# Performance work log

Hardware: AMD Instinct MI355X
Metric: run time of the kernel (lower is better)

The kernel has to match this reference:

```python
import jax, jax.numpy as jnp
import numpy as np

# Mamba2 defaults: d_model=256, d_state=64, d_conv=4, expand=2, headdim=64, ngroups=1
D_MODEL = 256
NB = 2            # num_blocks
D_STATE = 64
D_CONV = 4
D_INNER = 2 * D_MODEL          # 512
HEADDIM = 64
NHEADS = D_INNER // HEADDIM    # 8
CONV_DIM = D_INNER + 2 * D_STATE           # 640
D_IN_PROJ = 2 * D_INNER + 2 * D_STATE + NHEADS  # 1160
EPS = 1e-5


def setup_inputs() -> dict:
    key = jax.random.key(0)
    ks = jax.random.split(key, 10)
    x = jax.random.normal(ks[0], (8, 32, 32, D_MODEL), dtype=jnp.float32)
    in_proj_w = jax.random.normal(ks[1], (NB, D_IN_PROJ, D_MODEL), dtype=jnp.float32) * 0.02
    conv_w = jax.random.normal(ks[2], (NB, CONV_DIM, 1, D_CONV), dtype=jnp.float32) * 0.2
    conv_b = jax.random.normal(ks[3], (NB, CONV_DIM), dtype=jnp.float32) * 0.02
    dt_bias = jax.random.normal(ks[4], (NB, NHEADS), dtype=jnp.float32) * 0.5
    # A_log = log(A), A ~ U[1,16) as in mamba2 init
    A_log = jnp.log(jax.random.uniform(ks[5], (NB, NHEADS), minval=1.0, maxval=16.0, dtype=jnp.float32))
    D = jax.random.normal(ks[6], (NB, NHEADS), dtype=jnp.float32) * 0.1 + 1.0
    norm_w = jnp.ones((NB, D_INNER), dtype=jnp.float32)
    out_proj_w = jax.random.normal(ks[7], (NB, D_MODEL, D_INNER), dtype=jnp.float32) * 0.02
    return {"x": x, "in_proj_w": in_proj_w, "conv_w": conv_w, "conv_b": conv_b,
            "dt_bias": dt_bias, "A_log": A_log, "D": D, "norm_w": norm_w,
            "out_proj_w": out_proj_w}


def _mamba2_block(h, wi, cw, cb, dtb, a_log, d_skip, nw, wo):
    B, L, _ = h.shape
    zxbcdt = jnp.einsum('blc,pc->blp', h, wi)                 # (B,L,1160)
    z = zxbcdt[..., :D_INNER]                                 # (B,L,512)
    xBC = zxbcdt[..., D_INNER:D_INNER + CONV_DIM]             # (B,L,640)
    dt = jax.nn.softplus(zxbcdt[..., -NHEADS:] + dtb)         # (B,L,8)

    # causal depthwise conv1d, kernel 4, left pad 3
    xBC = jax.lax.conv_general_dilated(
        xBC.swapaxes(1, 2), cw, window_strides=(1,), padding=[(D_CONV - 1, 0)],
        dimension_numbers=('NCH', 'OIH', 'NCH'), feature_group_count=CONV_DIM)
    xBC = jax.nn.silu((xBC + cb[None, :, None]).swapaxes(1, 2))  # (B,L,640)

    xs = xBC[..., :D_INNER].reshape(B, L, NHEADS, HEADDIM)    # (B,L,h,p)
    Bm = xBC[..., D_INNER:D_INNER + D_STATE]                  # (B,L,s) ngroups=1
    Cm = xBC[..., D_INNER + D_STATE:]                         # (B,L,s)

    A = -jnp.exp(a_log)                                       # (h,)
    dA = jnp.exp(dt * A)                                      # (B,L,h)

    def step(s, inp):
        dA_t, dt_t, x_t, B_t, C_t = inp  # (B,h),(B,h),(B,h,p),(B,s),(B,s)
        s = s * dA_t[:, :, None, None] + (dt_t[:, :, None] * x_t)[..., None] * B_t[:, None, None, :]
        y = jnp.einsum('bhps,bs->bhp', s, C_t)
        return s, y

    s0 = jnp.zeros((B, NHEADS, HEADDIM, D_STATE), dtype=h.dtype)
    _, ys = jax.lax.scan(step, s0, (dA.swapaxes(0, 1), dt.swapaxes(0, 1),
                                    xs.swapaxes(0, 1), Bm.swapaxes(0, 1), Cm.swapaxes(0, 1)))
    y = ys.swapaxes(0, 1) + d_skip[:, None] * xs              # (B,L,h,p)
    y = y.reshape(B, L, D_INNER) * jax.nn.silu(z)             # gate
    y = y * jax.lax.rsqrt(jnp.mean(y * y, axis=-1, keepdims=True) + EPS) * nw  # gated RMSNorm
    return jnp.einsum('bld,cd->blc', y, wo)


def reference(x, in_proj_w, conv_w, conv_b, dt_bias, A_log, D, norm_w, out_proj_w):
    B, H, W, C = x.shape
    h = x.reshape(B, H * W, C)
    for i in range(NB):  # stacked blocks; Dropout is identity at inference
        h = _mamba2_block(h, in_proj_w[i], conv_w[i], conv_b[i], dt_bias[i],
                          A_log[i], D[i], norm_w[i], out_proj_w[i])
    return h.reshape(B, H, W, C)
```

## Files before the change

### kernel.cpp

```cpp
#include <hip/hip_runtime.h>
#include <hip/hip_bf16.h>
#include <math.h>

#define D_MODEL   256
#define D_STATE   64
#define D_CONV    4
#define D_INNER   512
#define HEADDIM   64
#define NHEADS    8
#define CONV_DIM  640
#define D_IN_PROJ 1160
#define ZXP       1280
#define SEQLEN    1024
#define BATCH     8
#define NROWS     8192
#define EPS       1e-5f
#define CHUNK     64
#define NCHUNK    (SEQLEN / CHUNK)

typedef __attribute__((ext_vector_type(8))) short bf16x8;
typedef __attribute__((ext_vector_type(4))) short s16x4;
typedef __attribute__((ext_vector_type(8))) unsigned short u16x8;
typedef __attribute__((ext_vector_type(4))) unsigned short u16x4;
typedef __attribute__((ext_vector_type(4))) float f32x4;
typedef unsigned int u32;
typedef unsigned short u16;

__device__ __forceinline__ void cp16(const short* g, short* l) {
    __builtin_amdgcn_global_load_lds((const __attribute__((address_space(1))) u32*)g,
                                     (__attribute__((address_space(3))) u32*)l, 16, 0, 0);
}
__device__ __forceinline__ u16 bfc(float f) {
    union { __hip_bfloat16 h; u16 u; } cv;
    cv.h = __float2bfloat16(f);
    return cv.u;
}
__device__ __forceinline__ float bf2f(u16 u) {
    union { u32 v; float f; } cv;
    cv.v = ((u32)u) << 16;
    return cv.f;
}
__device__ __forceinline__ void store_out(float* p, float v) { *p = v; }
__device__ __forceinline__ void store_out(__hip_bfloat16* p, float v) { *p = __float2bfloat16(v); }

__device__ __forceinline__ int swz(int row, int col) {
    return row * 64 + (((col & 56) ^ ((row & 7) << 3)) | (col & 7));
}
__device__ __forceinline__ bf16x8 ldfrag(const short* base, int row, int oct) {
    return *(const bf16x8*)&base[row * 64 + ((oct * 8) ^ ((row & 7) * 8))];
}
__device__ __forceinline__ void wr2u(short* base, int row, int col2, u16 a, u16 b) {
    int idx = row * 64 + (((col2 & 56) ^ ((row & 7) << 3)) | (col2 & 6));
    *(u32*)&base[idx] = (u32)a | ((u32)b << 16);
}

template <typename OUT, bool WITH_DT, bool SCALE>
__global__ __launch_bounds__(256) void gemm_mfma(const short* __restrict__ A,
                                                 const short* __restrict__ W,
                                                 OUT* __restrict__ C,
                                                 float* __restrict__ dtout,
                                                 const float* __restrict__ sc,
                                                 int N, int K, int lda) {
    __shared__ short As[128 * 32];
    __shared__ short Ws[128 * 32];
    const int tid  = threadIdx.x;
    const int m0   = blockIdx.y * 128;
    const int n0   = blockIdx.x * 128;
    const int wave = tid >> 6;
    const int lane = tid & 63;
    const int wm   = (wave & 1) * 64;
    const int wn   = (wave >> 1) * 64;
    const int lm   = lane & 15;
    const int lq   = lane >> 4;

    const int sr = tid >> 2;
    const int sk = (tid & 3) * 8;
    const short* ga = A + (size_t)(m0 + sr) * lda + sk;
    const short* gw = W + (size_t)(n0 + sr) * K + sk;
    short* la = &As[tid * 8];
    short* lw = &Ws[tid * 8];
    const size_t ga2 = (size_t)64 * lda;
    const size_t gw2 = (size_t)64 * K;

    f32x4 acc[4][4] = {};

    for (int k0 = 0; k0 < K; k0 += 32) {
        cp16(ga,       la);
        cp16(ga + ga2, la + 64 * 32);
        cp16(gw,       lw);
        cp16(gw + gw2, lw + 64 * 32);
        ga += 32; gw += 32;
        __syncthreads();
        bf16x8 af[4], bfr[4];
        #pragma unroll
        for (int i = 0; i < 4; i++) {
            af[i]  = *(const bf16x8*)&As[(wm + i * 16 + lm) * 32 + lq * 8];
            bfr[i] = *(const bf16x8*)&Ws[(wn + i * 16 + lm) * 32 + lq * 8];
        }
        #pragma unroll
        for (int i = 0; i < 4; i++)
            #pragma unroll
            for (int j = 0; j < 4; j++)
                acc[i][j] = __builtin_amdgcn_mfma_f32_16x16x32_bf16(af[i], bfr[j], acc[i][j], 0, 0, 0);
        __syncthreads();
    }
    #pragma unroll
    for (int i = 0; i < 4; i++)
        #pragma unroll
        for (int r = 0; r < 4; r++) {
            int m = m0 + wm + i * 16 + lq * 4 + r;
            float scl = SCALE ? rsqrtf(sc[m] * (1.f / (float)D_INNER) + EPS) : 1.f;
            #pragma unroll
            for (int j = 0; j < 4; j++) {
                int n = n0 + wn + j * 16 + lm;
                float v = acc[i][j][r];
                store_out(&C[(size_t)m * N + n], v * scl);
                if (WITH_DT) {
                    if (n >= D_IN_PROJ - NHEADS && n < D_IN_PROJ)
                        dtout[(size_t)m * NHEADS + (n - (D_IN_PROJ - NHEADS))] = v;
                }
            }
        }
}

#define NX_C  (NROWS * D_MODEL)
#define NWI_C (2 * ZXP * D_MODEL)
#define NWO_C (2 * D_MODEL * D_INNER)
__global__ __launch_bounds__(256) void cast_all_kernel(
    const float* __restrict__ x, const float* __restrict__ wi,
    const float* __restrict__ wo,
    u16* __restrict__ xb, u16* __restrict__ wib, u16* __restrict__ wob)
{
    int idx = blockIdx.x * 256 + threadIdx.x;
    if (idx < NX_C) { xb[idx] = bfc(x[idx]); return; }
    idx -= NX_C;
    if (idx < NWI_C) {
        int k = idx & 255;
        int rb = idx >> 8;
        int r = rb % ZXP;
        int blk = rb / ZXP;
        float v = (r < D_IN_PROJ)
            ? wi[(size_t)blk * D_IN_PROJ * D_MODEL + (size_t)r * D_MODEL + k] : 0.f;
        wib[idx] = bfc(v);
        return;
    }
    idx -= NWI_C;
    wob[idx] = bfc(wo[idx]);
}

__global__ __launch_bounds__(256) void conv_silu_kernel(const u16* __restrict__ zx,
                                                        const float* __restrict__ cw,
                                                        const float* __restrict__ cb,
                                                        u16* __restrict__ out) {
    int idx = blockIdx.x * 256 + threadIdx.x;
    int c4  = (idx % 160) * 4;
    int r4  = (idx / 160) * 4;
    int l4  = r4 & (SEQLEN - 1);
    float wt[4][4];
    #pragma unroll
    for (int k = 0; k < 4; k++)
        *(float4*)&wt[k][0] = *(const float4*)&cw[(c4 + k) * 4];
    float4 cbv = *(const float4*)&cb[c4];
    float cbk[4] = {cbv.x, cbv.y, cbv.z, cbv.w};

    const u16* base = zx + (size_t)r4 * ZXP + D_INNER + c4;
    u16x4 hrow[7];
    #pragma unroll
    for (int k = 0; k < 3; k++) {
        if (l4 != 0) hrow[k] = *(const u16x4*)&base[(k - 3) * ZXP];
        else { hrow[k][0] = 0; hrow[k][1] = 0; hrow[k][2] = 0; hrow[k][3] = 0; }
    }
    #pragma unroll
    for (int k = 3; k < 7; k++)
        hrow[k] = *(const u16x4*)&base[(k - 3) * ZXP];

    #pragma unroll
    for (int rr = 0; rr < 4; rr++) {
        u16x4 o;
        #pragma unroll
        for (int k = 0; k < 4; k++) {
            float acc = cbk[k];
            #pragma unroll
            for (int tap = 0; tap < 4; tap++)
                acc = fmaf(bf2f(hrow[rr + tap][k]), wt[k][tap], acc);
            float s = acc / (1.f + expf(-acc));
            o[k] = bfc(s);
        }
        *(u16x4*)&out[(size_t)(r4 + rr) * CONV_DIM + c4] = o;
    }
}

__global__ __launch_bounds__(256) void ssd_intra_kernel(
    const u16* __restrict__ xc, const float* __restrict__ dtbuf,
    const float* __restrict__ dt_bias, const float* __restrict__ A_log,
    u16* __restrict__ ys, u16* __restrict__ Schunk,
    float* __restrict__ adec, float* __restrict__ ssum)
{
    const int h   = blockIdx.x & 7;
    const int c   = (blockIdx.x >> 3) & 15;
    const int b   = blockIdx.x >> 7;
    const int tid = threadIdx.x;
    const int row0 = b * SEQLEN + c * CHUNK;

    if (tid < 8) ssum[blockIdx.x * 8 + tid] = 0.f;

    __shared__ short Xt[64 * 64];
    __shared__ short Bn[64 * 64];
    __shared__ short Cn[64 * 64];
    __shared__ short BTw[64 * 64];
    __shared__ float cums[64], dts_s[64], ws_s[64];

    if (tid < 64) {
        const float A = -expf(A_log[h]);
        float raw = dtbuf[(size_t)(row0 + tid) * NHEADS + h] + dt_bias[h];
        float dtv = (raw > 20.f) ? raw : log1pf(expf(raw));
        float v = dtv * A;
        #pragma unroll
        for (int off = 1; off < 64; off <<= 1) {
            float o = __shfl_up(v, off, 64);
            if (tid >= off) v += o;
        }
        float tot = __shfl(v, 63, 64);
        cums[tid]  = v;
        dts_s[tid] = dtv;
        ws_s[tid]  = expf(tot - v) * dtv;
        adec[(size_t)(b * NHEADS + h) * SEQLEN + c * CHUNK + tid] = expf(v);
    }
    __syncthreads();

    {
        const int t2 = (tid >> 3) * 2;
        const int c8 = (tid & 7) * 8;
        const u16* r0 = xc + (size_t)(row0 + t2) * CONV_DIM;
        const u16* r1 = r0 + CONV_DIM;
        u16x8 xv0 = *(const u16x8*)&r0[h * HEADDIM + c8];
        u16x8 xv1 = *(const u16x8*)&r1[h * HEADDIM + c8];
        u16x8 bv0 = *(const u16x8*)&r0[D_INNER + c8];
        u16x8 bv1 = *(const u16x8*)&r1[D_INNER + c8];
        u16x8 cv0 = *(const u16x8*)&r0[D_INNER + D_STATE + c8];
        u16x8 cv1 = *(const u16x8*)&r1[D_INNER + D_STATE + c8];
        *(u16x8*)&Bn[swz(t2,     c8)] = bv0;
        *(u16x8*)&Bn[swz(t2 + 1, c8)] = bv1;
        *(u16x8*)&Cn[swz(t2,     c8)] = cv0;
        *(u16x8*)&Cn[swz(t2 + 1, c8)] = cv1;
        float w0 = ws_s[t2], w1 = ws_s[t2 + 1];
        #pragma unroll
        for (int k = 0; k < 8; k++) {
            wr2u(Xt,  c8 + k, t2, xv0[k], xv1[k]);
            wr2u(BTw, c8 + k, t2, bfc(bf2f(bv0[k]) * w0), bfc(bf2f(bv1[k]) * w1));
        }
    }
    __syncthreads();

    const int lane = tid & 63, w = tid >> 6;
    const int lm = lane & 15, lq = lane >> 4;
    const int tau0 = 16 * w + lq * 4;

    bf16x8 aG0 = ldfrag(Bn, 16 * w + lm, lq);
    bf16x8 aG1 = ldfrag(Bn, 16 * w + lm, 4 + lq);
    f32x4 g[4] = {};
    #pragma unroll
    for (int j = 0; j < 4; j++) {
        g[j] = __builtin_amdgcn_mfma_f32_16x16x32_bf16(aG0, ldfrag(Cn, 16 * j + lm, lq),     g[j], 0, 0, 0);
        g[j] = __builtin_amdgcn_mfma_f32_16x16x32_bf16(aG1, ldfrag(Cn, 16 * j + lm, 4 + lq), g[j], 0, 0, 0);
    }
    float ctau[4], dtau[4];
    *(float4*)&ctau[0] = *(const float4*)&cums[tau0];
    *(float4*)&dtau[0] = *(const float4*)&dts_s[tau0];
    s16x4 mp[4];
    #pragma unroll
    for (int j = 0; j < 4; j++) {
        int t = 16 * j + lm;
        float ct = cums[t];
        #pragma unroll
        for (int r = 0; r < 4; r++) {
            int tau = tau0 + r;
            float m = (t >= tau) ? g[j][r] * __expf(ct - ctau[r]) * dtau[r] : 0.f;
            mp[j][r] = (short)bfc(m);
        }
    }
    __syncthreads();
    #pragma unroll
    for (int j = 0; j < 4; j++)
        *(s16x4*)&Cn[swz(16 * j + lm, tau0)] = mp[j];
    __syncthreads();

    bf16x8 aY0 = ldfrag(Cn,  16 * w + lm, lq);
    bf16x8 aY1 = ldfrag(Cn,  16 * w + lm, 4 + lq);
    bf16x8 aS0 = ldfrag(BTw, 16 * w + lm, lq);
    bf16x8 aS1 = ldfrag(BTw, 16 * w + lm, 4 + lq);
    f32x4 yv[4] = {}, sv[4] = {};
    #pragma unroll
    for (int j = 0; j < 4; j++) {
        bf16x8 xf0 = ldfrag(Xt, 16 * j + lm, lq);
        bf16x8 xf1 = ldfrag(Xt, 16 * j + lm, 4 + lq);
        yv[j] = __builtin_amdgcn_mfma_f32_16x16x32_bf16(aY0, xf0, yv[j], 0, 0, 0);
        yv[j] = __builtin_amdgcn_mfma_f32_16x16x32_bf16(aY1, xf1, yv[j], 0, 0, 0);
        sv[j] = __builtin_amdgcn_mfma_f32_16x16x32_bf16(aS0, xf0, sv[j], 0, 0, 0);
        sv[j] = __builtin_amdgcn_mfma_f32_16x16x32_bf16(aS1, xf1, sv[j], 0, 0, 0);
    }
    const int mrow = 16 * w + lq * 4;
    #pragma unroll
    for (int j = 0; j < 4; j++)
        #pragma unroll
        for (int r = 0; r < 4; r++)
            ys[(size_t)(row0 + mrow + r) * D_INNER + h * HEADDIM + 16 * j + lm] = bfc(yv[j][r]);
    u16* sb = Schunk + (size_t)((b * NCHUNK + c) * NHEADS + h) * 4096;
    #pragma unroll
    for (int j = 0; j < 4; j++)
        #pragma unroll
        for (int r = 0; r < 4; r++)
            sb[(mrow + r) * 64 + 16 * j + lm] = bfc(sv[j][r]);
}

__global__ __launch_bounds__(256) void ssd_state_scan_kernel(
    u16* __restrict__ Schunk, const float* __restrict__ adec)
{
    const int q  = blockIdx.x & 3;
    const int bh = blockIdx.x >> 2;
    const int b  = bh >> 3, h = bh & 7;
    const int base = q * 1024 + threadIdx.x * 4;

    u16x4 v[NCHUNK];
    float atot[NCHUNK];
    #pragma unroll
    for (int c = 0; c < NCHUNK; c++) {
        v[c] = *(const u16x4*)&Schunk[(size_t)((b * NCHUNK + c) * NHEADS + h) * 4096 + base];
        atot[c] = adec[(size_t)bh * SEQLEN + c * CHUNK + 63];
    }
    float run[4] = {0.f, 0.f, 0.f, 0.f};
    #pragma unroll
    for (int c = 0; c < NCHUNK; c++) {
        u16x4 pv;
        #pragma unroll
        for (int k = 0; k < 4; k++) pv[k] = bfc(run[k]);
        *(u16x4*)&Schunk[(size_t)((b * NCHUNK + c) * NHEADS + h) * 4096 + base] = pv;
        #pragma unroll
        for (int k = 0; k < 4; k++)
            run[k] = fmaf(atot[c], run[k], bf2f(v[c][k]));
    }
}

__global__ __launch_bounds__(128) void ssd_finish_kernel(
    const u16* __restrict__ xc, const u16* __restrict__ zx,
    const u16* __restrict__ Schunk, const float* __restrict__ adec,
    const float* __restrict__ Dp, const float* __restrict__ nw,
    u16* __restrict__ ys, float* __restrict__ ssum)
{
    const int hp   = blockIdx.x & 3;
    const int half = (blockIdx.x >> 2) & 1;
    const int c    = (blockIdx.x >> 3) & 15;
    const int b    = blockIdx.x >> 7;
    const int h0   = hp * 2;
    const int tid  = threadIdx.x;
    const int row0 = b * SEQLEN + c * CHUNK + half * 32;

    __shared__ short Ct[32 * 64];
    __shared__ short STs[64 * 64];
    __shared__ float a_s[64];
    __shared__ float nw_s[128];

    {
        int t2 = (tid >> 3) * 2, n8 = (tid & 7) * 8;
        const u16* r0 = xc + (size_t)(row0 + t2) * CONV_DIM + D_INNER + D_STATE;
        u16x8 v0 = *(const u16x8*)&r0[n8];
        u16x8 v1 = *(const u16x8*)&r0[CONV_DIM + n8];
        *(u16x8*)&Ct[swz(t2,     n8)] = v0;
        *(u16x8*)&Ct[swz(t2 + 1, n8)] = v1;
        if (tid < 16) {
            int hh = tid >> 3, t4 = (tid & 7) * 4;
            *(float4*)&a_s[hh * 32 + t4] = *(const float4*)
                &adec[(size_t)(b * NHEADS + h0 + hh) * SEQLEN + c * CHUNK + half * 32 + t4];
        }
        nw_s[tid] = nw[h0 * 64 + tid];
    }

    const int lane = tid & 63, w = tid >> 6;
    const int lm = lane & 15, lq = lane >> 4;
    const int trow = 16 * w + lq * 4;

    bf16x8 aC0, aC1;
    float ss[4] = {0.f, 0.f, 0.f, 0.f};

    for (int hi = 0; hi < 2; hi++) {
        const int h = h0 + hi;
        {
            const u16* sb = Schunk + (size_t)((b * NCHUNK + c) * NHEADS + h) * 4096;
            int n4 = (tid >> 3) * 4, p8 = (tid & 7) * 8;
            u16x8 s0 = *(const u16x8*)&sb[(n4 + 0) * 64 + p8];
            u16x8 s1 = *(const u16x8*)&sb[(n4 + 1) * 64 + p8];
            u16x8 s2 = *(const u16x8*)&sb[(n4 + 2) * 64 + p8];
            u16x8 s3 = *(const u16x8*)&sb[(n4 + 3) * 64 + p8];
            #pragma unroll
            for (int k = 0; k < 8; k++) {
                wr2u(STs, p8 + k, n4,     s0[k], s1[k]);
                wr2u(STs, p8 + k, n4 + 2, s2[k], s3[k]);
            }
        }
        __syncthreads();
        if (hi == 0) {
            aC0 = ldfrag(Ct, 16 * w + lm, lq);
            aC1 = ldfrag(Ct, 16 * w + lm, 4 + lq);
        }
        f32x4 U[4] = {};
        #pragma unroll
        for (int j = 0; j < 4; j++) {
            U[j] = __builtin_amdgcn_mfma_f32_16x16x32_bf16(aC0, ldfrag(STs, 16 * j + lm, lq),     U[j], 0, 0, 0);
            U[j] = __builtin_amdgcn_mfma_f32_16x16x32_bf16(aC1, ldfrag(STs, 16 * j + lm, 4 + lq), U[j], 0, 0, 0);
        }
        float Dh = Dp[h];
        #pragma unroll
        for (int j = 0; j < 4; j++) {
            int col = h * 64 + 16 * j + lm;
            float nwv = nw_s[hi * 64 + 16 * j + lm];
            #pragma unroll
            for (int r = 0; r < 4; r++) {
                int row = trow + r;
                size_t grow = (size_t)(row0 + row);
                float a = a_s[hi * 32 + row];
                float u = U[j][r] * a
                        + bf2f(ys[grow * D_INNER + col])
                        + Dh * bf2f(xc[grow * CONV_DIM + col]);
                float zv = bf2f(zx[grow * ZXP + col]);
                float gt = zv / (1.f + expf(-zv));
                float v = u * gt;
                ss[r] = fmaf(v, v, ss[r]);
                ys[grow * D_INNER + col] = bfc(v * nwv);
            }
        }
        __syncthreads();
    }
    #pragma unroll
    for (int r = 0; r < 4; r++) {
        float s = ss[r];
        s += __shfl_xor(s, 1, 64); s += __shfl_xor(s, 2, 64);
        s += __shfl_xor(s, 4, 64); s += __shfl_xor(s, 8, 64);
        if (lm == 0)
            atomicAdd(&ssum[row0 + trow + r], s);
    }
}

extern "C" void kernel_launch(void* const* d_in, const int* in_sizes, int n_in,
                              void* d_out, int out_size, void* d_ws, size_t ws_size,
                              hipStream_t stream) {
    const float* x          = (const float*)d_in[0];
    const float* in_proj_w  = (const float*)d_in[1];
    const float* conv_w     = (const float*)d_in[2];
    const float* conv_b     = (const float*)d_in[3];
    const float* dt_bias    = (const float*)d_in[4];
    const float* A_log      = (const float*)d_in[5];
    const float* Dp         = (const float*)d_in[6];
    const float* norm_w     = (const float*)d_in[7];
    const float* out_proj_w = (const float*)d_in[8];
    float* out = (float*)d_out;

    u16*   buf_zx = (u16*)d_ws;
    u16*   buf_xc = buf_zx + (size_t)NROWS * ZXP;
    u16*   buf_ys = buf_xc + (size_t)NROWS * CONV_DIM;
    u16*   buf_S  = buf_ys + (size_t)NROWS * D_INNER;
    u16*   buf_hb = buf_S  + (size_t)BATCH * NCHUNK * NHEADS * 4096;
    u16*   buf_wi = buf_hb + (size_t)NROWS * D_MODEL;
    u16*   buf_wo = buf_wi + (size_t)2 * ZXP * D_MODEL;
    float* buf_dt = (float*)(buf_wo + (size_t)2 * D_MODEL * D_INNER);
    float* buf_a  = buf_dt + (size_t)NROWS * NHEADS;
    float* buf_sc = buf_a  + (size_t)BATCH * NHEADS * SEQLEN;

    cast_all_kernel<<<(NX_C + NWI_C + NWO_C) / 256, 256, 0, stream>>>(
        x, in_proj_w, out_proj_w, buf_hb, buf_wi, buf_wo);

    for (int i = 0; i < 2; i++) {
        gemm_mfma<__hip_bfloat16, true, false><<<dim3(ZXP / 128, NROWS / 128), 256, 0, stream>>>(
            (const short*)buf_hb, (const short*)(buf_wi + (size_t)i * ZXP * D_MODEL),
            (__hip_bfloat16*)buf_zx, buf_dt, nullptr, ZXP, D_MODEL, D_MODEL);

        conv_silu_kernel<<<(NROWS / 4) * 160 / 256, 256, 0, stream>>>(
            buf_zx, conv_w + (size_t)i * CONV_DIM * D_CONV,
            conv_b + (size_t)i * CONV_DIM, buf_xc);

        ssd_intra_kernel<<<BATCH * NCHUNK * NHEADS, 256, 0, stream>>>(
            buf_xc, buf_dt, dt_bias + i * NHEADS, A_log + i * NHEADS,
            buf_ys, buf_S, buf_a, buf_sc);

        ssd_state_scan_kernel<<<BATCH * NHEADS * 4, 256, 0, stream>>>(buf_S, buf_a);

        ssd_finish_kernel<<<BATCH * NCHUNK * 2 * 4, 128, 0, stream>>>(
            buf_xc, buf_zx, buf_S, buf_a, Dp + i * NHEADS,
            norm_w + (size_t)i * D_INNER, buf_ys, buf_sc);

        if (i == 0) {
            gemm_mfma<__hip_bfloat16, false, true><<<dim3(D_MODEL / 128, NROWS / 128), 256, 0, stream>>>(
                (const short*)buf_ys, (const short*)buf_wo,
                (__hip_bfloat16*)buf_hb, nullptr, buf_sc, D_MODEL, D_INNER, D_INNER);
        } else {
            gemm_mfma<float, false, true><<<dim3(D_MODEL / 128, NROWS / 128), 256, 0, stream>>>(
                (const short*)buf_ys, (const short*)(buf_wo + (size_t)D_MODEL * D_INNER),
                out, nullptr, buf_sc, D_MODEL, D_INNER, D_INNER);
        }
    }
}
```

Measured before the change: 206.2 us.

## Fuse causal conv+SiLU into SSD intra-chunk kernel and fold D skip there

Removes the standalone conv_silu kernel. The SSD intra kernel now loads raw xBC rows from the in_proj output, applies the depthwise causal conv, bias and SiLU itself, and writes only the C projection to a small buffer for the finish kernel. The D*x skip term is added in the intra kernel from shared memory, so the finish kernel no longer rereads the conv output. This saves one launch plus a full write and reread of the 640-wide conv buffer. In exchange the B and C channels are recomputed by every head block (8x redundant conv work) and each block does more global loads.

```diff
diff --git a/kernel.cpp b/kernel.cpp
--- a/kernel.cpp
+++ b/kernel.cpp
@@ -148,53 +148,14 @@
     wob[idx] = bfc(wo[idx]);
 }
 
-__global__ __launch_bounds__(256) void conv_silu_kernel(const u16* __restrict__ zx,
-                                                        const float* __restrict__ cw,
-                                                        const float* __restrict__ cb,
-                                                        u16* __restrict__ out) {
-    int idx = blockIdx.x * 256 + threadIdx.x;
-    int c4  = (idx % 160) * 4;
-    int r4  = (idx / 160) * 4;
-    int l4  = r4 & (SEQLEN - 1);
-    float wt[4][4];
-    #pragma unroll
-    for (int k = 0; k < 4; k++)
-        *(float4*)&wt[k][0] = *(const float4*)&cw[(c4 + k) * 4];
-    float4 cbv = *(const float4*)&cb[c4];
-    float cbk[4] = {cbv.x, cbv.y, cbv.z, cbv.w};
-
-    const u16* base = zx + (size_t)r4 * ZXP + D_INNER + c4;
-    u16x4 hrow[7];
-    #pragma unroll
-    for (int k = 0; k < 3; k++) {
-        if (l4 != 0) hrow[k] = *(const u16x4*)&base[(k - 3) * ZXP];
-        else { hrow[k][0] = 0; hrow[k][1] = 0; hrow[k][2] = 0; hrow[k][3] = 0; }
-    }
-    #pragma unroll
-    for (int k = 3; k < 7; k++)
-        hrow[k] = *(const u16x4*)&base[(k - 3) * ZXP];
-
-    #pragma unroll
-    for (int rr = 0; rr < 4; rr++) {
-        u16x4 o;
-        #pragma unroll
-        for (int k = 0; k < 4; k++) {
-            float acc = cbk[k];
-            #pragma unroll
-            for (int tap = 0; tap < 4; tap++)
-                acc = fmaf(bf2f(hrow[rr + tap][k]), wt[k][tap], acc);
-            float s = acc / (1.f + expf(-acc));
-            o[k] = bfc(s);
-        }
-        *(u16x4*)&out[(size_t)(r4 + rr) * CONV_DIM + c4] = o;
-    }
-}
-
 __global__ __launch_bounds__(256) void ssd_intra_kernel(
-    const u16* __restrict__ xc, const float* __restrict__ dtbuf,
+    const u16* __restrict__ zx, const float* __restrict__ dtbuf,
     const float* __restrict__ dt_bias, const float* __restrict__ A_log,
+    const float* __restrict__ cw, const float* __restrict__ cb,
+    const float* __restrict__ Dp,
     u16* __restrict__ ys, u16* __restrict__ Schunk,
-    float* __restrict__ adec, float* __restrict__ ssum)
+    float* __restrict__ adec, float* __restrict__ ssum,
+    u16* __restrict__ Cb)
 {
     const int h   = blockIdx.x & 7;
     const int c   = (blockIdx.x >> 3) & 15;
@@ -209,6 +170,8 @@
     __shared__ short Cn[64 * 64];
     __shared__ short BTw[64 * 64];
     __shared__ float cums[64], dts_s[64], ws_s[64];
+    __shared__ float4 wls[192];
+    __shared__ float  bls[192];
 
     if (tid < 64) {
         const float A = -expf(A_log[h]);
@@ -225,29 +188,70 @@
         dts_s[tid] = dtv;
         ws_s[tid]  = expf(tot - v) * dtv;
         adec[(size_t)(b * NHEADS + h) * SEQLEN + c * CHUNK + tid] = expf(v);
+    } else {
+        int wi = tid - 64;
+        int g = wi >> 6, k = wi & 63;
+        int ch = (g == 0) ? h * HEADDIM + k : (g == 1 ? 512 + k : 576 + k);
+        wls[wi] = *(const float4*)&cw[ch * 4];
+        bls[wi] = cb[ch];
     }
     __syncthreads();
 
     {
         const int t2 = (tid >> 3) * 2;
         const int c8 = (tid & 7) * 8;
-        const u16* r0 = xc + (size_t)(row0 + t2) * CONV_DIM;
-        const u16* r1 = r0 + CONV_DIM;
-        u16x8 xv0 = *(const u16x8*)&r0[h * HEADDIM + c8];
-        u16x8 xv1 = *(const u16x8*)&r1[h * HEADDIM + c8];
-        u16x8 bv0 = *(const u16x8*)&r0[D_INNER + c8];
-        u16x8 bv1 = *(const u16x8*)&r1[D_INNER + c8];
-        u16x8 cv0 = *(const u16x8*)&r0[D_INNER + D_STATE + c8];
-        u16x8 cv1 = *(const u16x8*)&r1[D_INNER + D_STATE + c8];
-        *(u16x8*)&Bn[swz(t2,     c8)] = bv0;
-        *(u16x8*)&Bn[swz(t2 + 1, c8)] = bv1;
-        *(u16x8*)&Cn[swz(t2,     c8)] = cv0;
-        *(u16x8*)&Cn[swz(t2 + 1, c8)] = cv1;
-        float w0 = ws_s[t2], w1 = ws_s[t2 + 1];
-        #pragma unroll
-        for (int k = 0; k < 8; k++) {
-            wr2u(Xt,  c8 + k, t2, xv0[k], xv1[k]);
-            wr2u(BTw, c8 + k, t2, bfc(bf2f(bv0[k]) * w0), bfc(bf2f(bv1[k]) * w1));
+        const int lb = c * CHUNK + t2;
+        const u16* zb = zx + (size_t)(row0 + t2) * ZXP + D_INNER;
+        const float w0 = ws_s[t2], w1 = ws_s[t2 + 1];
+        u16x8 zz;
+        #pragma unroll
+        for (int q = 0; q < 8; q++) zz[q] = 0;
+
+        #pragma unroll
+        for (int g = 0; g < 3; g++) {
+            const int gc = (g == 0) ? h * HEADDIM + c8 : (g == 1 ? 512 + c8 : 576 + c8);
+            const u16* p = zb + gc;
+            u16x8 r0 = (lb >= 3) ? *(const u16x8*)(p - 3 * ZXP) : zz;
+            u16x8 r1 = (lb >= 2) ? *(const u16x8*)(p - 2 * ZXP) : zz;
+            u16x8 r2 = (lb >= 1) ? *(const u16x8*)(p - 1 * ZXP) : zz;
+            u16x8 r3 = *(const u16x8*)p;
+            u16x8 r4 = *(const u16x8*)(p + ZXP);
+            u16x8 o0, o1;
+            #pragma unroll
+            for (int k = 0; k < 8; k++) {
+                float4 w4  = wls[g * 64 + c8 + k];
+                float bias = bls[g * 64 + c8 + k];
+                float a0 = bias, a1 = bias;
+                a0 = fmaf(bf2f(r0[k]), w4.x, a0);
+                a0 = fmaf(bf2f(r1[k]), w4.y, a0);
+                a0 = fmaf(bf2f(r2[k]), w4.z, a0);
+                a0 = fmaf(bf2f(r3[k]), w4.w, a0);
+                a1 = fmaf(bf2f(r1[k]), w4.x, a1);
+                a1 = fmaf(bf2f(r2[k]), w4.y, a1);
+                a1 = fmaf(bf2f(r3[k]), w4.z, a1);
+                a1 = fmaf(bf2f(r4[k]), w4.w, a1);
+                float s0 = a0 / (1.f + expf(-a0));
+                float s1 = a1 / (1.f + expf(-a1));
+                if (g == 0) {
+                    wr2u(Xt, c8 + k, t2, bfc(s0), bfc(s1));
+                } else if (g == 1) {
+                    o0[k] = bfc(s0); o1[k] = bfc(s1);
+                    wr2u(BTw, c8 + k, t2, bfc(s0 * w0), bfc(s1 * w1));
+                } else {
+                    o0[k] = bfc(s0); o1[k] = bfc(s1);
+                }
+            }
+            if (g == 1) {
+                *(u16x8*)&Bn[swz(t2,     c8)] = o0;
+                *(u16x8*)&Bn[swz(t2 + 1, c8)] = o1;
+            } else if (g == 2) {
+                *(u16x8*)&Cn[swz(t2,     c8)] = o0;
+                *(u16x8*)&Cn[swz(t2 + 1, c8)] = o1;
+                if (h == 0) {
+                    *(u16x8*)&Cb[(size_t)(row0 + t2)     * 64 + c8] = o0;
+                    *(u16x8*)&Cb[(size_t)(row0 + t2 + 1) * 64 + c8] = o1;
+                }
+            }
         }
     }
     __syncthreads();
@@ -299,12 +303,16 @@
         sv[j] = __builtin_amdgcn_mfma_f32_16x16x32_bf16(aS0, xf0, sv[j], 0, 0, 0);
         sv[j] = __builtin_amdgcn_mfma_f32_16x16x32_bf16(aS1, xf1, sv[j], 0, 0, 0);
     }
+    const float Dh = Dp[h];
     const int mrow = 16 * w + lq * 4;
     #pragma unroll
     for (int j = 0; j < 4; j++)
         #pragma unroll
-        for (int r = 0; r < 4; r++)
-            ys[(size_t)(row0 + mrow + r) * D_INNER + h * HEADDIM + 16 * j + lm] = bfc(yv[j][r]);
+        for (int r = 0; r < 4; r++) {
+            float xv = bf2f((u16)Xt[swz(16 * j + lm, mrow + r)]);
+            ys[(size_t)(row0 + mrow + r) * D_INNER + h * HEADDIM + 16 * j + lm]
+                = bfc(yv[j][r] + Dh * xv);
+        }
     u16* sb = Schunk + (size_t)((b * NCHUNK + c) * NHEADS + h) * 4096;
     #pragma unroll
     for (int j = 0; j < 4; j++)
@@ -342,9 +350,9 @@
 }
 
 __global__ __launch_bounds__(128) void ssd_finish_kernel(
-    const u16* __restrict__ xc, const u16* __restrict__ zx,
+    const u16* __restrict__ Cb, const u16* __restrict__ zx,
     const u16* __restrict__ Schunk, const float* __restrict__ adec,
-    const float* __restrict__ Dp, const float* __restrict__ nw,
+    const float* __restrict__ nw,
     u16* __restrict__ ys, float* __restrict__ ssum)
 {
     const int hp   = blockIdx.x & 3;
@@ -362,9 +370,9 @@
 
     {
         int t2 = (tid >> 3) * 2, n8 = (tid & 7) * 8;
-        const u16* r0 = xc + (size_t)(row0 + t2) * CONV_DIM + D_INNER + D_STATE;
+        const u16* r0 = Cb + (size_t)(row0 + t2) * 64;
         u16x8 v0 = *(const u16x8*)&r0[n8];
-        u16x8 v1 = *(const u16x8*)&r0[CONV_DIM + n8];
+        u16x8 v1 = *(const u16x8*)&r0[64 + n8];
         *(u16x8*)&Ct[swz(t2,     n8)] = v0;
         *(u16x8*)&Ct[swz(t2 + 1, n8)] = v1;
         if (tid < 16) {
@@ -408,7 +416,6 @@
             U[j] = __builtin_amdgcn_mfma_f32_16x16x32_bf16(aC0, ldfrag(STs, 16 * j + lm, lq),     U[j], 0, 0, 0);
             U[j] = __builtin_amdgcn_mfma_f32_16x16x32_bf16(aC1, ldfrag(STs, 16 * j + lm, 4 + lq), U[j], 0, 0, 0);
         }
-        float Dh = Dp[h];
         #pragma unroll
         for (int j = 0; j < 4; j++) {
             int col = h * 64 + 16 * j + lm;
@@ -418,9 +425,7 @@
                 int row = trow + r;
                 size_t grow = (size_t)(row0 + row);
                 float a = a_s[hi * 32 + row];
-                float u = U[j][r] * a
-                        + bf2f(ys[grow * D_INNER + col])
-                        + Dh * bf2f(xc[grow * CONV_DIM + col]);
+                float u = U[j][r] * a + bf2f(ys[grow * D_INNER + col]);
                 float zv = bf2f(zx[grow * ZXP + col]);
                 float gt = zv / (1.f + expf(-zv));
                 float v = u * gt;
@@ -455,8 +460,8 @@
     float* out = (float*)d_out;
 
     u16*   buf_zx = (u16*)d_ws;
-    u16*   buf_xc = buf_zx + (size_t)NROWS * ZXP;
-    u16*   buf_ys = buf_xc + (size_t)NROWS * CONV_DIM;
+    u16*   buf_cb = buf_zx + (size_t)NROWS * ZXP;
+    u16*   buf_ys = buf_cb + (size_t)NROWS * 64;
     u16*   buf_S  = buf_ys + (size_t)NROWS * D_INNER;
     u16*   buf_hb = buf_S  + (size_t)BATCH * NCHUNK * NHEADS * 4096;
     u16*   buf_wi = buf_hb + (size_t)NROWS * D_MODEL;
@@ -473,18 +478,16 @@
             (const short*)buf_hb, (const short*)(buf_wi + (size_t)i * ZXP * D_MODEL),
             (__hip_bfloat16*)buf_zx, buf_dt, nullptr, ZXP, D_MODEL, D_MODEL);
 
-        conv_silu_kernel<<<(NROWS / 4) * 160 / 256, 256, 0, stream>>>(
-            buf_zx, conv_w + (size_t)i * CONV_DIM * D_CONV,
-            conv_b + (size_t)i * CONV_DIM, buf_xc);
-
         ssd_intra_kernel<<<BATCH * NCHUNK * NHEADS, 256, 0, stream>>>(
-            buf_xc, buf_dt, dt_bias + i * NHEADS, A_log + i * NHEADS,
-            buf_ys, buf_S, buf_a, buf_sc);
+            buf_zx, buf_dt, dt_bias + i * NHEADS, A_log + i * NHEADS,
+            conv_w + (size_t)i * CONV_DIM * D_CONV, conv_b + (size_t)i * CONV_DIM,
+            Dp + i * NHEADS,
+            buf_ys, buf_S, buf_a, buf_sc, buf_cb);
 
         ssd_state_scan_kernel<<<BATCH * NHEADS * 4, 256, 0, stream>>>(buf_S, buf_a);
 
         ssd_finish_kernel<<<BATCH * NCHUNK * 2 * 4, 128, 0, stream>>>(
-            buf_xc, buf_zx, buf_S, buf_a, Dp + i * NHEADS,
+            buf_cb, buf_zx, buf_S, buf_a,
             norm_w + (size_t)i * D_INNER, buf_ys, buf_sc);
 
         if (i == 0) {
```

After: 213.7 us. 1.04x slower.
